# Kernel optimization log

Hardware: AMD Instinct MI355X
Metric: run time of the kernel (lower is better)

The kernel has to match this reference:

```python
import jax, jax.numpy as jnp
import numpy as np

NUM_HEADS = 16
ROPE_BASE = 10000.0


def _rope_cos_sin(seq_len, head_dim, dtype):
    inv_freq = 1.0 / (ROPE_BASE ** (jnp.arange(0, head_dim, 2, dtype=jnp.float32) / head_dim))
    freqs = jnp.arange(seq_len, dtype=jnp.float32)[:, None] * inv_freq[None, :]  # [L, hd/2]
    return jnp.cos(freqs).astype(dtype), jnp.sin(freqs).astype(dtype)


def _apply_rope(t, cos, sin):
    # t: [B, H, L, hd]; cos/sin: [L, hd/2] broadcast over B,H
    x1 = t[..., ::2]
    x2 = t[..., 1::2]
    r1 = x1 * cos - x2 * sin
    r2 = x1 * sin + x2 * cos
    return jnp.stack([r1, r2], axis=-1).reshape(t.shape)


def setup_inputs() -> dict:
    key = jax.random.key(0)
    k1, k2, k3 = jax.random.split(key, 3)
    B, L, D = 2, 2048, 1024
    x = jax.random.normal(k1, (B, L, D), dtype=jnp.float32)
    W_qkv = jax.random.normal(k2, (3 * D, D), dtype=jnp.float32) * (D ** -0.5)
    W_out = jax.random.normal(k3, (D, D), dtype=jnp.float32) * (D ** -0.5)
    return {"x": x, "W_qkv": W_qkv, "W_out": W_out}


def reference(x, W_qkv, W_out):
    B, L, D = x.shape
    H = NUM_HEADS
    hd = D // H
    scale = hd ** -0.5

    qkv = x @ W_qkv.T                              # [B, L, 3D]
    qkv = qkv.reshape(B, L, 3, H, hd)
    qkv = jnp.transpose(qkv, (2, 0, 3, 1, 4))      # [3, B, H, L, hd]
    q, k, v = qkv[0], qkv[1], qkv[2]

    cos, sin = _rope_cos_sin(L, hd, x.dtype)
    q = _apply_rope(q, cos, sin)
    k = _apply_rope(k, cos, sin)

    logits = jnp.einsum("bhqd,bhkd->bhqk", q, k) * scale
    attn = jax.nn.softmax(logits, axis=-1)         # dropout p=0.0 -> identity
    out = jnp.einsum("bhqk,bhkd->bhqd", attn, v)   # [B, H, L, hd]
    out = jnp.transpose(out, (0, 2, 1, 3)).reshape(B, L, D)
    return out @ W_out.T
```

## Files before the change

### kernel.cpp

```cpp
#include <hip/hip_runtime.h>
#include <hip/hip_bf16.h>
#include <stdint.h>


typedef __bf16 bf16x8 __attribute__((ext_vector_type(8)));
typedef __bf16 bf16x4v __attribute__((ext_vector_type(4)));
typedef float f32x4 __attribute__((ext_vector_type(4)));

__device__ __forceinline__ unsigned short f2bf(float f) {
  union { float f; unsigned int u; } v; v.f = f;
  unsigned int r = v.u + 0x7FFFu + ((v.u >> 16) & 1u);
  return (unsigned short)(r >> 16);
}
__device__ __forceinline__ float b2f(unsigned short u) {
  union { unsigned int u; float f; } v; v.u = ((unsigned int)u) << 16;
  return v.f;
}

__device__ __forceinline__ void gl2lds16(const void* gptr, void* lptr) {
  __builtin_amdgcn_global_load_lds(
      (const __attribute__((address_space(1))) unsigned int*)gptr,
      (__attribute__((address_space(3))) unsigned int*)lptr, 16, 0, 0);
}

__global__ void cvt_all(const float4* __restrict__ x,
                        const float4* __restrict__ wq,
                        const float4* __restrict__ wo,
                        ushort4* __restrict__ xb,
                        ushort4* __restrict__ wqb,
                        ushort4* __restrict__ wob) {
  int i = blockIdx.x * 256 + threadIdx.x;
  float4 v; ushort4* dst; int j;
  if (i < 1048576)      { v = x[i];            dst = xb;  j = i; }
  else if (i < 1835008) { v = wq[i - 1048576]; dst = wqb; j = i - 1048576; }
  else                  { v = wo[i - 1835008]; dst = wob; j = i - 1835008; }
  ushort4 o;
  o.x = f2bf(v.x); o.y = f2bf(v.y); o.z = f2bf(v.z); o.w = f2bf(v.w);
  dst[j] = o;
}

template<int OUT_BF16>
__global__ __launch_bounds__(256) void gemm_bt(
    const __hip_bfloat16* __restrict__ A,
    const __hip_bfloat16* __restrict__ B,
    void* __restrict__ C, int M, int N, int K) {
  __shared__ __align__(16) __hip_bfloat16 As[128 * 32];
  __shared__ __align__(16) __hip_bfloat16 Bs[128 * 32];
  const int tid = threadIdx.x;
  const int lane = tid & 63;
  const int wave = tid >> 6;
  const int wm = (wave >> 1) * 64, wn = (wave & 1) * 64;
  const int g = lane >> 4, lr = lane & 15;
  const int m0 = blockIdx.y * 128, n0 = blockIdx.x * 128;
  f32x4 acc[4][4] = {};

  const char* Ag = (const char*)(A + (size_t)m0 * K);
  const char* Bg = (const char*)(B + (size_t)n0 * K);
  const size_t ldb = (size_t)K * 2;

  for (int kt = 0; kt < K; kt += 32) {
    const char* Ak = Ag + (size_t)kt * 2;
    const char* Bk = Bg + (size_t)kt * 2;
#pragma unroll
    for (int j = 0; j < 2; ++j) {
      int c = tid + j * 256;
      int row = c >> 2;
      int colb = (c & 3) * 16;
      gl2lds16(Ak + (size_t)row * ldb + colb, (char*)As + c * 16);
      gl2lds16(Bk + (size_t)row * ldb + colb, (char*)Bs + c * 16);
    }
    asm volatile("s_waitcnt vmcnt(0)" ::: "memory");
    __syncthreads();
    bf16x8 af[4], bfr[4];
#pragma unroll
    for (int i = 0; i < 4; ++i)
      af[i] = *(const bf16x8*)((const char*)As + (size_t)(wm + i * 16 + lr) * 64 + g * 16);
#pragma unroll
    for (int i = 0; i < 4; ++i)
      bfr[i] = *(const bf16x8*)((const char*)Bs + (size_t)(wn + i * 16 + lr) * 64 + g * 16);
#pragma unroll
    for (int i = 0; i < 4; ++i)
#pragma unroll
      for (int j = 0; j < 4; ++j)
        acc[i][j] = __builtin_amdgcn_mfma_f32_16x16x32_bf16(af[i], bfr[j], acc[i][j], 0, 0, 0);
    __syncthreads();
  }

#pragma unroll
  for (int i = 0; i < 4; ++i) {
#pragma unroll
    for (int j = 0; j < 4; ++j) {
      int n = n0 + wn + j * 16 + lr;
#pragma unroll
      for (int r = 0; r < 4; ++r) {
        int m = m0 + wm + i * 16 + g * 4 + r;
        float v = acc[i][j][r];
        if (OUT_BF16) {
          ((unsigned short*)C)[(size_t)m * N + n] = f2bf(v);
        } else {
          ((float*)C)[(size_t)m * N + n] = v;
        }
      }
    }
  }
}

__global__ void rope_scatter(const __hip_bfloat16* __restrict__ qkv,
                             __hip_bfloat16* __restrict__ Qs,
                             __hip_bfloat16* __restrict__ Ks,
                             __hip_bfloat16* __restrict__ Vt) {
  const int t = blockIdx.x * 256 + threadIdx.x;
  const int i = t & 31;
  const int lc = (t >> 5) & 255;
  const int h = (t >> 13) & 15;
  const int b = t >> 17;
  const float inv_freq = powf(10000.0f, -(float)i * (1.0f / 32.0f));
  const float QSCALE = 0.125f * 1.44269504088896f;
  const unsigned short* qk = (const unsigned short*)qkv;
  unsigned short v0[8], v1[8];
#pragma unroll
  for (int j = 0; j < 8; ++j) {
    const int l = lc * 8 + j;
    const size_t row = ((size_t)(b * 2048 + l)) * 3072;
    float s, c;
    sincosf((float)l * inv_freq, &s, &c);
    ushort2 qp = *(const ushort2*)(qk + row + h * 64 + 2 * i);
    ushort2 kp = *(const ushort2*)(qk + row + 1024 + h * 64 + 2 * i);
    ushort2 vp = *(const ushort2*)(qk + row + 2048 + h * 64 + 2 * i);
    float x1 = b2f(qp.x), x2 = b2f(qp.y);
    float y1 = b2f(kp.x), y2 = b2f(kp.y);
    size_t oidx = (((size_t)(b * 16 + h)) * 2048 + l) * 64 + 2 * i;
    ushort2 qo, ko;
    qo.x = f2bf((x1 * c - x2 * s) * QSCALE);
    qo.y = f2bf((x1 * s + x2 * c) * QSCALE);
    ko.x = f2bf(y1 * c - y2 * s);
    ko.y = f2bf(y1 * s + y2 * c);
    *(ushort2*)((unsigned short*)Qs + oidx) = qo;
    *(ushort2*)((unsigned short*)Ks + oidx) = ko;
    v0[j] = vp.x; v1[j] = vp.y;
  }
  unsigned short* Vtu = (unsigned short*)Vt;
  const size_t vrow0 = (((size_t)(b * 16 + h)) * 64 + 2 * i) * 2048 + lc * 8;
  const size_t vrow1 = vrow0 + 2048;
  *(ushort4*)(Vtu + vrow0)     = make_ushort4(v0[0], v0[1], v0[2], v0[3]);
  *(ushort4*)(Vtu + vrow0 + 4) = make_ushort4(v0[4], v0[5], v0[6], v0[7]);
  *(ushort4*)(Vtu + vrow1)     = make_ushort4(v1[0], v1[1], v1[2], v1[3]);
  *(ushort4*)(Vtu + vrow1 + 4) = make_ushort4(v1[4], v1[5], v1[6], v1[7]);
}

__global__ __launch_bounds__(512, 4) void attn_fwd(
    const __hip_bfloat16* __restrict__ Qs,
    const __hip_bfloat16* __restrict__ Ks,
    const __hip_bfloat16* __restrict__ Vt,
    float* __restrict__ Opart,
    float2* __restrict__ Ml) {
  constexpr int L = 2048;
  extern __shared__ __align__(16) char lds[];
  const int tid = threadIdx.x, lane = tid & 63, w = tid >> 6;
  const int g = lane >> 4, lr = lane & 15;
  const int blk = blockIdx.x;
  const int xcd = blk & 7, slot = blk >> 3;
  const int bh = xcd * 4 + (slot >> 4);
  const int rem = slot & 15;
  const int qt = rem >> 1, half = rem & 1;
  const int q0 = qt * 256 + w * 32 + lr;
  const int kt0 = half * 16;

  const __hip_bfloat16* Qr = Qs + ((size_t)bh * L + q0) * 64;
  bf16x8 qf[2][2];
  qf[0][0] = *(const bf16x8*)(Qr + g * 8);
  qf[0][1] = *(const bf16x8*)(Qr + 32 + g * 8);
  qf[1][0] = *(const bf16x8*)(Qr + 16 * 64 + g * 8);
  qf[1][1] = *(const bf16x8*)(Qr + 16 * 64 + 32 + g * 8);

  const int xmask = (lr & 7) << 4;
  const int loff0 = ((g * 16) ^ (xmask & 0x30)) + (xmask & 0x40);
  const int loff1 = loff0 ^ 64;
  const int kb0 = lr * 128 + loff0;
  const int kb1 = lr * 128 + loff1;
  char* Pme = lds + 32768 + w * 4096 + lr * 128;
  const int pwoff = (g * 8) ^ (xmask & 0x10);
  const int pm = xmask & 0x60;

  const int c0 = tid * 16;
  const int os = c0 ^ (((c0 >> 7) & 7) << 4);
  const char* Ksrc = (const char*)(Ks + (size_t)bh * L * 64) + (size_t)kt0 * 8192 + os;
  const char* Vsrc = (const char*)(Vt + (size_t)bh * 64 * L) +
                     (size_t)(os >> 7) * (L * 2) + kt0 * 128 + (os & 127);

  auto stage = [&](int bo) {
    gl2lds16(Ksrc, lds + bo + c0);
    gl2lds16(Vsrc, lds + 16384 + bo + c0);
    Ksrc += 8192; Vsrc += 128;
  };

  f32x4 oacc[2][4] = {};
  float mrun[2] = {-1e30f, -1e30f}, lpart[2] = {0.0f, 0.0f};

  stage(0);

  for (int kt = 0; kt < 16; ++kt) {
    const int bo = (kt & 1) * 8192;
    if (kt + 1 < 16) {
      stage(bo ^ 8192);
      asm volatile("s_waitcnt vmcnt(2)" ::: "memory");
    } else {
      asm volatile("s_waitcnt vmcnt(0)" ::: "memory");
    }
    asm volatile("s_barrier" ::: "memory");

    const char* Kc = lds + bo;
    const char* Vc = lds + 16384 + bo;

    f32x4 sacc[2][4] = {};
#pragma unroll
    for (int mf = 0; mf < 4; ++mf) {
      bf16x8 a0 = *(const bf16x8*)(Kc + kb0 + mf * 2048);
      bf16x8 a1 = *(const bf16x8*)(Kc + kb1 + mf * 2048);
      sacc[0][mf] = __builtin_amdgcn_mfma_f32_16x16x32_bf16(a0, qf[0][0], sacc[0][mf], 0, 0, 0);
      sacc[0][mf] = __builtin_amdgcn_mfma_f32_16x16x32_bf16(a1, qf[0][1], sacc[0][mf], 0, 0, 0);
      sacc[1][mf] = __builtin_amdgcn_mfma_f32_16x16x32_bf16(a0, qf[1][0], sacc[1][mf], 0, 0, 0);
      sacc[1][mf] = __builtin_amdgcn_mfma_f32_16x16x32_bf16(a1, qf[1][1], sacc[1][mf], 0, 0, 0);
    }

#pragma unroll
    for (int qg = 0; qg < 2; ++qg) {
      float t0 = fmaxf(fmaxf(sacc[qg][0][0], sacc[qg][0][1]), fmaxf(sacc[qg][0][2], sacc[qg][0][3]));
      float t1 = fmaxf(fmaxf(sacc[qg][1][0], sacc[qg][1][1]), fmaxf(sacc[qg][1][2], sacc[qg][1][3]));
      float t2 = fmaxf(fmaxf(sacc[qg][2][0], sacc[qg][2][1]), fmaxf(sacc[qg][2][2], sacc[qg][2][3]));
      float t3 = fmaxf(fmaxf(sacc[qg][3][0], sacc[qg][3][1]), fmaxf(sacc[qg][3][2], sacc[qg][3][3]));
      float tmax = fmaxf(fmaxf(t0, t1), fmaxf(t2, t3));
      tmax = fmaxf(tmax, __shfl_xor(tmax, 16));
      tmax = fmaxf(tmax, __shfl_xor(tmax, 32));
      if (__any(tmax > mrun[qg] + 8.0f)) {
        float mnew = fmaxf(mrun[qg], tmax);
        float al = __builtin_amdgcn_exp2f(mrun[qg] - mnew);
        mrun[qg] = mnew;
        lpart[qg] *= al;
#pragma unroll
        for (int d = 0; d < 4; ++d) oacc[qg][d] = oacc[qg][d] * al;
      }
#pragma unroll
      for (int mf = 0; mf < 4; ++mf) {
        float p0 = __builtin_amdgcn_exp2f(sacc[qg][mf][0] - mrun[qg]);
        float p1 = __builtin_amdgcn_exp2f(sacc[qg][mf][1] - mrun[qg]);
        float p2 = __builtin_amdgcn_exp2f(sacc[qg][mf][2] - mrun[qg]);
        float p3 = __builtin_amdgcn_exp2f(sacc[qg][mf][3] - mrun[qg]);
        lpart[qg] += (p0 + p1) + (p2 + p3);
        bf16x4v pk = { (__bf16)p0, (__bf16)p1, (__bf16)p2, (__bf16)p3 };
        *(bf16x4v*)(Pme + qg * 2048 + pwoff + ((mf * 32) ^ pm)) = pk;
      }
    }

#pragma unroll
    for (int ks = 0; ks < 2; ++ks) {
      const int lo = ks ? loff1 : loff0;
      bf16x8 pf0 = *(const bf16x8*)(Pme + lo);
      bf16x8 pf1 = *(const bf16x8*)(Pme + 2048 + lo);
#pragma unroll
      for (int df = 0; df < 4; ++df) {
        bf16x8 a = *(const bf16x8*)(Vc + (ks ? kb1 : kb0) + df * 2048);
        oacc[0][df] = __builtin_amdgcn_mfma_f32_16x16x32_bf16(a, pf0, oacc[0][df], 0, 0, 0);
        oacc[1][df] = __builtin_amdgcn_mfma_f32_16x16x32_bf16(a, pf1, oacc[1][df], 0, 0, 0);
      }
    }
    asm volatile("s_waitcnt lgkmcnt(0)" ::: "memory");
    __builtin_amdgcn_sched_barrier(0);
    asm volatile("s_barrier" ::: "memory");
  }

#pragma unroll
  for (int qg = 0; qg < 2; ++qg) {
    float lsum = lpart[qg];
    lsum += __shfl_xor(lsum, 16);
    lsum += __shfl_xor(lsum, 32);
    const size_t rowi = ((size_t)bh * L + q0 + qg * 16) * 2 + half;
    float* Od = Opart + rowi * 64;
#pragma unroll
    for (int df = 0; df < 4; ++df)
      *(f32x4*)(Od + df * 16 + g * 4) = oacc[qg][df];
    if (g == 0) {
      float2 ml; ml.x = mrun[qg]; ml.y = lsum;
      Ml[rowi] = ml;
    }
  }
}

__global__ __launch_bounds__(256) void attn_reduce(
    const float* __restrict__ Opart, const float2* __restrict__ Ml,
    unsigned short* __restrict__ Ob) {
  int t = blockIdx.x * 256 + threadIdx.x;
  int d = t & 63;
  int r = t >> 6;
  float2 a = Ml[2 * r], b = Ml[2 * r + 1];
  float m = fmaxf(a.x, b.x);
  float w0 = __builtin_amdgcn_exp2f(a.x - m);
  float w1 = __builtin_amdgcn_exp2f(b.x - m);
  float l = a.y * w0 + b.y * w1;
  float o = Opart[(size_t)(2 * r) * 64 + d] * w0 + Opart[(size_t)(2 * r + 1) * 64 + d] * w1;
  float out = o / l;
  int bh = r >> 11, qq = r & 2047;
  Ob[(((size_t)(bh >> 4) * 2048 + qq)) * 1024 + (bh & 15) * 64 + d] = f2bf(out);
}

extern "C" void kernel_launch(void* const* d_in, const int* in_sizes, int n_in,
                              void* d_out, int out_size, void* d_ws, size_t ws_size,
                              hipStream_t stream) {
  (void)in_sizes; (void)n_in; (void)out_size; (void)ws_size;
  const float* x    = (const float*)d_in[0];
  const float* wqkv = (const float*)d_in[1];
  const float* wout = (const float*)d_in[2];

  char* ws = (char*)d_ws;
  auto* wob   = (__hip_bfloat16*)(ws + ((size_t)0u  << 20));
  auto* Qsb   = (__hip_bfloat16*)(ws + ((size_t)2u  << 20));
  auto* Ob    = (__hip_bfloat16*)(ws + ((size_t)2u  << 20));
  auto* Ksb   = (__hip_bfloat16*)(ws + ((size_t)10u << 20));
  auto* Vtb   = (__hip_bfloat16*)(ws + ((size_t)18u << 20));
  auto* qkvb  = (__hip_bfloat16*)(ws + ((size_t)26u << 20));
  auto* Opart = (float*)         (ws + ((size_t)26u << 20));
  auto* xb    = (__hip_bfloat16*)(ws + ((size_t)50u << 20));
  auto* wqb   = (__hip_bfloat16*)(ws + ((size_t)58u << 20));
  auto* Mlp   = (float2*)        (ws + ((size_t)58u << 20));

  cvt_all<<<8192, 256, 0, stream>>>((const float4*)x, (const float4*)wqkv,
                                    (const float4*)wout,
                                    (ushort4*)xb, (ushort4*)wqb, (ushort4*)wob);
  gemm_bt<1><<<dim3(24, 32), 256, 0, stream>>>(xb, wqb, (void*)qkvb, 4096, 3072, 1024);
  rope_scatter<<<1024, 256, 0, stream>>>(qkvb, Qsb, Ksb, Vtb);
  attn_fwd<<<512, 512, 65536, stream>>>(Qsb, Ksb, Vtb, Opart, Mlp);
  attn_reduce<<<16384, 256, 0, stream>>>(Opart, Mlp, (unsigned short*)Ob);
  gemm_bt<0><<<dim3(8, 32), 256, 0, stream>>>(Ob, wob, d_out, 4096, 1024, 1024);
}
```

Baseline: 147.0 us.

## Keep softmax probabilities in registers via permuted V layout, shrink attention blocks

Permutes the V-transpose column order in rope_scatter so the S accumulator layout of the QK^T MFMA directly matches the B-operand layout needed for PV. This removes the LDS round-trip for P: no write and re-read of probabilities, and no P scratch region. The attention kernel moves to 256-thread blocks with static 32KB LDS and twice as many blocks, each thread issuing two async loads per tile. s_setprio is added around the MFMA sections. The change depends on the permuted V layout exactly matching the MFMA register layout, and the smaller blocks mean less K/V reuse per block.

```diff
diff --git a/kernel.cpp b/kernel.cpp
--- a/kernel.cpp
+++ b/kernel.cpp
@@ -4,7 +4,6 @@
 
 
 typedef __bf16 bf16x8 __attribute__((ext_vector_type(8)));
-typedef __bf16 bf16x4v __attribute__((ext_vector_type(4)));
 typedef float f32x4 __attribute__((ext_vector_type(4)));
 
 __device__ __forceinline__ unsigned short f2bf(float f) {
@@ -139,31 +138,33 @@
     *(ushort2*)((unsigned short*)Ks + oidx) = ko;
     v0[j] = vp.x; v1[j] = vp.y;
   }
+  const int m = lc & 3;
+  const int colA = ((m & 1) << 4) + ((m >> 1) << 2);
   unsigned short* Vtu = (unsigned short*)Vt;
-  const size_t vrow0 = (((size_t)(b * 16 + h)) * 64 + 2 * i) * 2048 + lc * 8;
+  const size_t vrow0 = (((size_t)(b * 16 + h)) * 64 + 2 * i) * 2048 + (lc >> 2) * 32;
   const size_t vrow1 = vrow0 + 2048;
-  *(ushort4*)(Vtu + vrow0)     = make_ushort4(v0[0], v0[1], v0[2], v0[3]);
-  *(ushort4*)(Vtu + vrow0 + 4) = make_ushort4(v0[4], v0[5], v0[6], v0[7]);
-  *(ushort4*)(Vtu + vrow1)     = make_ushort4(v1[0], v1[1], v1[2], v1[3]);
-  *(ushort4*)(Vtu + vrow1 + 4) = make_ushort4(v1[4], v1[5], v1[6], v1[7]);
-}
-
-__global__ __launch_bounds__(512, 4) void attn_fwd(
+  *(ushort4*)(Vtu + vrow0 + colA)     = make_ushort4(v0[0], v0[1], v0[2], v0[3]);
+  *(ushort4*)(Vtu + vrow0 + colA + 8) = make_ushort4(v0[4], v0[5], v0[6], v0[7]);
+  *(ushort4*)(Vtu + vrow1 + colA)     = make_ushort4(v1[0], v1[1], v1[2], v1[3]);
+  *(ushort4*)(Vtu + vrow1 + colA + 8) = make_ushort4(v1[4], v1[5], v1[6], v1[7]);
+}
+
+__global__ __launch_bounds__(256, 4) void attn_fwd(
     const __hip_bfloat16* __restrict__ Qs,
     const __hip_bfloat16* __restrict__ Ks,
     const __hip_bfloat16* __restrict__ Vt,
     float* __restrict__ Opart,
     float2* __restrict__ Ml) {
   constexpr int L = 2048;
-  extern __shared__ __align__(16) char lds[];
+  __shared__ __align__(16) char lds[32768];
   const int tid = threadIdx.x, lane = tid & 63, w = tid >> 6;
   const int g = lane >> 4, lr = lane & 15;
   const int blk = blockIdx.x;
   const int xcd = blk & 7, slot = blk >> 3;
-  const int bh = xcd * 4 + (slot >> 4);
-  const int rem = slot & 15;
+  const int bh = xcd * 4 + (slot >> 5);
+  const int rem = slot & 31;
   const int qt = rem >> 1, half = rem & 1;
-  const int q0 = qt * 256 + w * 32 + lr;
+  const int q0 = qt * 128 + w * 32 + lr;
   const int kt0 = half * 16;
 
   const __hip_bfloat16* Qr = Qs + ((size_t)bh * L + q0) * 64;
@@ -175,23 +176,25 @@
 
   const int xmask = (lr & 7) << 4;
   const int loff0 = ((g * 16) ^ (xmask & 0x30)) + (xmask & 0x40);
-  const int loff1 = loff0 ^ 64;
   const int kb0 = lr * 128 + loff0;
-  const int kb1 = lr * 128 + loff1;
-  char* Pme = lds + 32768 + w * 4096 + lr * 128;
-  const int pwoff = (g * 8) ^ (xmask & 0x10);
-  const int pm = xmask & 0x60;
-
-  const int c0 = tid * 16;
-  const int os = c0 ^ (((c0 >> 7) & 7) << 4);
-  const char* Ksrc = (const char*)(Ks + (size_t)bh * L * 64) + (size_t)kt0 * 8192 + os;
-  const char* Vsrc = (const char*)(Vt + (size_t)bh * 64 * L) +
-                     (size_t)(os >> 7) * (L * 2) + kt0 * 128 + (os & 127);
+  const int kb1 = kb0 ^ 64;
+
+  const int c0 = tid * 16, c1 = c0 + 4096;
+  const int os0 = c0 ^ (((c0 >> 7) & 7) << 4);
+  const int os1 = c1 ^ (((c1 >> 7) & 7) << 4);
+  const char* Kb = (const char*)(Ks + (size_t)bh * L * 64) + (size_t)kt0 * 8192;
+  const char* Vb = (const char*)(Vt + (size_t)bh * 64 * L) + kt0 * 128;
+  const char* KsrcA = Kb + os0;
+  const char* KsrcB = Kb + os1;
+  const char* VsrcA = Vb + (size_t)(os0 >> 7) * (L * 2) + (os0 & 127);
+  const char* VsrcB = Vb + (size_t)(os1 >> 7) * (L * 2) + (os1 & 127);
 
   auto stage = [&](int bo) {
-    gl2lds16(Ksrc, lds + bo + c0);
-    gl2lds16(Vsrc, lds + 16384 + bo + c0);
-    Ksrc += 8192; Vsrc += 128;
+    gl2lds16(KsrcA, lds + bo + c0);
+    gl2lds16(KsrcB, lds + bo + c1);
+    gl2lds16(VsrcA, lds + 16384 + bo + c0);
+    gl2lds16(VsrcB, lds + 16384 + bo + c1);
+    KsrcA += 8192; KsrcB += 8192; VsrcA += 128; VsrcB += 128;
   };
 
   f32x4 oacc[2][4] = {};
@@ -203,16 +206,17 @@
     const int bo = (kt & 1) * 8192;
     if (kt + 1 < 16) {
       stage(bo ^ 8192);
-      asm volatile("s_waitcnt vmcnt(2)" ::: "memory");
+      asm volatile("s_waitcnt vmcnt(4)" ::: "memory");
     } else {
       asm volatile("s_waitcnt vmcnt(0)" ::: "memory");
     }
-    asm volatile("s_barrier" ::: "memory");
+    __builtin_amdgcn_s_barrier();
 
     const char* Kc = lds + bo;
     const char* Vc = lds + 16384 + bo;
 
     f32x4 sacc[2][4] = {};
+    __builtin_amdgcn_s_setprio(1);
 #pragma unroll
     for (int mf = 0; mf < 4; ++mf) {
       bf16x8 a0 = *(const bf16x8*)(Kc + kb0 + mf * 2048);
@@ -222,6 +226,7 @@
       sacc[1][mf] = __builtin_amdgcn_mfma_f32_16x16x32_bf16(a0, qf[1][0], sacc[1][mf], 0, 0, 0);
       sacc[1][mf] = __builtin_amdgcn_mfma_f32_16x16x32_bf16(a1, qf[1][1], sacc[1][mf], 0, 0, 0);
     }
+    __builtin_amdgcn_s_setprio(0);
 
 #pragma unroll
     for (int qg = 0; qg < 2; ++qg) {
@@ -247,26 +252,34 @@
         float p2 = __builtin_amdgcn_exp2f(sacc[qg][mf][2] - mrun[qg]);
         float p3 = __builtin_amdgcn_exp2f(sacc[qg][mf][3] - mrun[qg]);
         lpart[qg] += (p0 + p1) + (p2 + p3);
-        bf16x4v pk = { (__bf16)p0, (__bf16)p1, (__bf16)p2, (__bf16)p3 };
-        *(bf16x4v*)(Pme + qg * 2048 + pwoff + ((mf * 32) ^ pm)) = pk;
+        sacc[qg][mf][0] = p0; sacc[qg][mf][1] = p1;
+        sacc[qg][mf][2] = p2; sacc[qg][mf][3] = p3;
       }
     }
 
 #pragma unroll
     for (int ks = 0; ks < 2; ++ks) {
-      const int lo = ks ? loff1 : loff0;
-      bf16x8 pf0 = *(const bf16x8*)(Pme + lo);
-      bf16x8 pf1 = *(const bf16x8*)(Pme + 2048 + lo);
+      bf16x8 pf[2];
+#pragma unroll
+      for (int qg = 0; qg < 2; ++qg) {
+#pragma unroll
+        for (int j = 0; j < 4; ++j) {
+          pf[qg][j]     = (__bf16)sacc[qg][2 * ks][j];
+          pf[qg][4 + j] = (__bf16)sacc[qg][2 * ks + 1][j];
+        }
+      }
+      const int kb = ks ? kb1 : kb0;
+      __builtin_amdgcn_s_setprio(1);
 #pragma unroll
       for (int df = 0; df < 4; ++df) {
-        bf16x8 a = *(const bf16x8*)(Vc + (ks ? kb1 : kb0) + df * 2048);
-        oacc[0][df] = __builtin_amdgcn_mfma_f32_16x16x32_bf16(a, pf0, oacc[0][df], 0, 0, 0);
-        oacc[1][df] = __builtin_amdgcn_mfma_f32_16x16x32_bf16(a, pf1, oacc[1][df], 0, 0, 0);
-      }
+        bf16x8 a = *(const bf16x8*)(Vc + kb + df * 2048);
+        oacc[0][df] = __builtin_amdgcn_mfma_f32_16x16x32_bf16(a, pf[0], oacc[0][df], 0, 0, 0);
+        oacc[1][df] = __builtin_amdgcn_mfma_f32_16x16x32_bf16(a, pf[1], oacc[1][df], 0, 0, 0);
+      }
+      __builtin_amdgcn_s_setprio(0);
     }
     asm volatile("s_waitcnt lgkmcnt(0)" ::: "memory");
-    __builtin_amdgcn_sched_barrier(0);
-    asm volatile("s_barrier" ::: "memory");
+    __builtin_amdgcn_s_barrier();
   }
 
 #pragma unroll
@@ -328,7 +341,7 @@
                                     (ushort4*)xb, (ushort4*)wqb, (ushort4*)wob);
   gemm_bt<1><<<dim3(24, 32), 256, 0, stream>>>(xb, wqb, (void*)qkvb, 4096, 3072, 1024);
   rope_scatter<<<1024, 256, 0, stream>>>(qkvb, Qsb, Ksb, Vtb);
-  attn_fwd<<<512, 512, 65536, stream>>>(Qsb, Ksb, Vtb, Opart, Mlp);
+  attn_fwd<<<1024, 256, 0, stream>>>(Qsb, Ksb, Vtb, Opart, Mlp);
   attn_reduce<<<16384, 256, 0, stream>>>(Opart, Mlp, (unsigned short*)Ob);
   gemm_bt<0><<<dim3(8, 32), 256, 0, stream>>>(Ob, wob, d_out, 4096, 1024, 1024);
 }
```

After: 147.1 us. About the same (+0.1%).
